# Performance work log

Hardware: AMD Instinct MI355X
Metric: run time of the kernel (lower is better)

## Reference

```python
import jax, jax.numpy as jnp
import numpy as np

B, T, D, U = 256, 2048, 64, 64


def setup_inputs() -> dict:
    key = jax.random.key(0)
    k1, k2, k3 = jax.random.split(key, 3)
    x = jax.random.normal(k1, (B, T, D), dtype=jnp.float32)
    Wx = jax.random.normal(k2, (D, 4 * U), dtype=jnp.float32) * 0.05
    Wh = jax.random.normal(k3, (U, 4 * U), dtype=jnp.float32) * 0.05
    b = jnp.zeros((4 * U,), dtype=jnp.float32)
    return {"x": x, "Wx": Wx, "Wh": Wh, "b": b}


def reference(x, Wx, Wh, b):
    # Keras LSTM gate order: i, f, g(candidate), o; act=tanh, rec_act=sigmoid.
    u = Wh.shape[0]
    # Precompute the input projection for all timesteps (same math, vectorized).
    xz = jnp.einsum('btd,dg->btg', x, Wx) + b  # [B, T, 4U]

    def step(carry, zt):
        h, c = carry                       # [B, U] each
        z = zt + h @ Wh                    # [B, 4U]
        i = jax.nn.sigmoid(z[:, :u])
        f = jax.nn.sigmoid(z[:, u:2 * u])
        g = jnp.tanh(z[:, 2 * u:3 * u])
        o = jax.nn.sigmoid(z[:, 3 * u:])
        c_new = f * c + i * g
        h_new = o * jnp.tanh(c_new)
        return (h_new, c_new), (c_new, h_new)

    h0 = jnp.zeros((x.shape[0], u), dtype=x.dtype)
    c0 = jnp.zeros((x.shape[0], u), dtype=x.dtype)
    _, (cs, hs) = jax.lax.scan(step, (h0, c0), jnp.swapaxes(xz, 0, 1))
    cs = jnp.swapaxes(cs, 0, 1)  # [B, T, U]
    hs = jnp.swapaxes(hs, 0, 1)  # [B, T, U]
    return jnp.concatenate([cs, hs], axis=-1)  # [B, T, 2U], cell states first
```

## Files before the change

### kernel.cpp

```cpp
#include <hip/hip_runtime.h>
#include <stdint.h>


#define T_STEPS 2048
#define DIM     64
#define GATES   256
#define CHUNK   16
#define NCHUNK  (T_STEPS / CHUNK)

typedef _Float16 f16;
typedef _Float16 f16x8 __attribute__((ext_vector_type(8)));
typedef float    f32x4 __attribute__((ext_vector_type(4)));

__device__ __forceinline__ void sync_lds() {
    __builtin_amdgcn_sched_barrier(0);
    asm volatile("s_waitcnt lgkmcnt(0)" ::: "memory");
    __builtin_amdgcn_sched_barrier(0);
    __builtin_amdgcn_s_barrier();
    __builtin_amdgcn_sched_barrier(0);
}

__device__ __forceinline__ float sigm(float z) {
    return __builtin_amdgcn_rcpf(1.f + __expf(-z));
}

#define MFMA16(A, B, C) __builtin_amdgcn_mfma_f32_16x16x32_f16(A, B, C, 0, 0, 0)

__device__ __forceinline__ void pack8(f16x8& d, const float4& a, const float4& b) {
    d[0]=(f16)a.x; d[1]=(f16)a.y; d[2]=(f16)a.z; d[3]=(f16)a.w;
    d[4]=(f16)b.x; d[5]=(f16)b.y; d[6]=(f16)b.z; d[7]=(f16)b.w;
}

__global__ __launch_bounds__(256, 1)
void lstm_r13_kernel(const float* __restrict__ x,
                     const float* __restrict__ Wx,
                     const float* __restrict__ Wh,
                     const float* __restrict__ bias,
                     float* __restrict__ out)
{
    __shared__ __align__(16) f16   sH[2][64];
    __shared__ __align__(16) float sXZ[4][CHUNK][16][4];

    const int tid  = threadIdx.x;
    const int lane = tid & 63;
    const int w    = tid >> 6;
    const int j    = lane & 15;
    const int g    = lane >> 4;
    const int u    = w * 16 + j;

    const int batch = blockIdx.x;
    const float* xb = x + (size_t)batch * T_STEPS * DIM;
    float* ob = out + (size_t)batch * T_STEPS * (2 * DIM);

    f16x8 Bh[4][2], Bx[4][2];
    f32x4 bias4[4];
#pragma unroll
    for (int q = 0; q < 4; ++q) {
        const int col = q * 64 + u;
        const float bb = bias[col];
        bias4[q][0] = bb; bias4[q][1] = bb; bias4[q][2] = bb; bias4[q][3] = bb;
#pragma unroll
        for (int ks = 0; ks < 2; ++ks)
#pragma unroll
            for (int e = 0; e < 8; ++e) {
                const int k = ks * 32 + g * 8 + e;
                Bh[q][ks][e] = (f16)Wh[k * GATES + col];
                Bx[q][ks][e] = (f16)Wx[k * GATES + col];
            }
    }
    const f32x4 zero4 = {0.f, 0.f, 0.f, 0.f};

    if (tid < 128) sH[tid >> 6][tid & 63] = (f16)0.f;

    float4 x0, x1, x2, x3;
    {
        const float* xr = xb + (size_t)j * DIM + g * 8;
        x0 = *(const float4*)(xr);      x1 = *(const float4*)(xr + 4);
        x2 = *(const float4*)(xr + 32); x3 = *(const float4*)(xr + 36);
    }

    float c = 0.f;
    __syncthreads();

#pragma unroll 1
    for (int n = 0; n < NCHUNK; ++n) {
        f16x8 ax0, ax1;
        pack8(ax0, x0, x1); pack8(ax1, x2, x3);
        f32x4 z0 = MFMA16(ax0, Bx[0][0], bias4[0]); z0 = MFMA16(ax1, Bx[0][1], z0);
        f32x4 z1 = MFMA16(ax0, Bx[1][0], bias4[1]); z1 = MFMA16(ax1, Bx[1][1], z1);
        f32x4 z2 = MFMA16(ax0, Bx[2][0], bias4[2]); z2 = MFMA16(ax1, Bx[2][1], z2);
        f32x4 z3 = MFMA16(ax0, Bx[3][0], bias4[3]); z3 = MFMA16(ax1, Bx[3][1], z3);
#pragma unroll
        for (int r = 0; r < 4; ++r) {
            float4 v = {z0[r], z1[r], z2[r], z3[r]};
            *(float4*)&sXZ[w][4 * g + r][j][0] = v;
        }
        asm volatile("s_waitcnt lgkmcnt(0)" ::: "memory");

        if (n + 1 < NCHUNK) {
            const float* xr = xb + ((size_t)(n + 1) * CHUNK + j) * DIM + g * 8;
            x0 = *(const float4*)(xr);      x1 = *(const float4*)(xr + 4);
            x2 = *(const float4*)(xr + 32); x3 = *(const float4*)(xr + 36);
        }

#pragma unroll
        for (int s = 0; s < CHUNK; ++s) {
            const int pb = s & 1;
            float4 xzv = *(const float4*)&sXZ[w][s][j][0];
            f16x8 A0 = *(const f16x8*)&sH[pb][g * 8];
            f16x8 A1 = *(const f16x8*)&sH[pb][32 + g * 8];

            f32x4 h0 = MFMA16(A0, Bh[0][0], zero4); h0 = MFMA16(A1, Bh[0][1], h0);
            f32x4 h1 = MFMA16(A0, Bh[1][0], zero4); h1 = MFMA16(A1, Bh[1][1], h1);
            f32x4 h2 = MFMA16(A0, Bh[2][0], zero4); h2 = MFMA16(A1, Bh[2][1], h2);
            f32x4 h3 = MFMA16(A0, Bh[3][0], zero4); h3 = MFMA16(A1, Bh[3][1], h3);

            float zi = h0[0] + xzv.x, zf = h1[0] + xzv.y;
            float zg = h2[0] + xzv.z, zo = h3[0] + xzv.w;
            float gi = sigm(zi), gf = sigm(zf), go = sigm(zo);
            float gg = fmaf(2.f, sigm(zg + zg), -1.f);
            c = fmaf(gf, c, gi * gg);
            float e2 = __expf(-2.f * fabsf(c));
            float th = copysignf(
                fmaf(-2.f, e2 * __builtin_amdgcn_rcpf(1.f + e2), 1.f), c);
            float hh = go * th;

            const size_t t = (size_t)n * CHUNK + s;
            if (g == 2)      sH[pb ^ 1][u] = (f16)hh;
            else if (g == 0) ob[t * 128 + u]      = c;
            else if (g == 1) ob[t * 128 + 64 + u] = hh;
            sync_lds();
        }
    }
}

extern "C" void kernel_launch(void* const* d_in, const int* in_sizes, int n_in,
                              void* d_out, int out_size, void* d_ws, size_t ws_size,
                              hipStream_t stream) {
    const float* x  = (const float*)d_in[0];
    const float* Wx = (const float*)d_in[1];
    const float* Wh = (const float*)d_in[2];
    const float* b  = (const float*)d_in[3];
    float* out = (float*)d_out;

    hipLaunchKernelGGL(lstm_r13_kernel, dim3(256), dim3(256), 0, stream,
                       x, Wx, Wh, b, out);
}
```

Measured before the change: 586.1 us.

## Run each batch LSTM on a single wavefront to drop per-step barriers

Collapses the four-wave block into one 64-lane wave per batch row. That wave computes all 16 gate tiles of the recurrent matmul itself, keeping the Wh fragments in registers and the Wx fragments in LDS. Because only one wave is involved, the per-timestep LDS barrier disappears, and each lane selects its gate values with a lane-dependent pick. The cost is four times more serial MFMA work per step on a single wave and only one wave per CU to hide latency.

```diff
diff --git a/kernel.cpp b/kernel.cpp
--- a/kernel.cpp
+++ b/kernel.cpp
@@ -12,14 +12,6 @@
 typedef _Float16 f16x8 __attribute__((ext_vector_type(8)));
 typedef float    f32x4 __attribute__((ext_vector_type(4)));
 
-__device__ __forceinline__ void sync_lds() {
-    __builtin_amdgcn_sched_barrier(0);
-    asm volatile("s_waitcnt lgkmcnt(0)" ::: "memory");
-    __builtin_amdgcn_sched_barrier(0);
-    __builtin_amdgcn_s_barrier();
-    __builtin_amdgcn_sched_barrier(0);
-}
-
 __device__ __forceinline__ float sigm(float z) {
     return __builtin_amdgcn_rcpf(1.f + __expf(-z));
 }
@@ -31,46 +23,56 @@
     d[4]=(f16)b.x; d[5]=(f16)b.y; d[6]=(f16)b.z; d[7]=(f16)b.w;
 }
 
-__global__ __launch_bounds__(256, 1)
-void lstm_r13_kernel(const float* __restrict__ x,
+__device__ __forceinline__ float pick4(int m, float A0, float A1, float A2, float A3) {
+    float r  = (m & 1) ? A1 : A0;
+    float sx = (m & 1) ? A3 : A2;
+    return (m & 2) ? sx : r;
+}
+
+__global__ __attribute__((amdgpu_flat_work_group_size(64, 64),
+                          amdgpu_waves_per_eu(1, 1)))
+void lstm_r14_kernel(const float* __restrict__ x,
                      const float* __restrict__ Wx,
                      const float* __restrict__ Wh,
                      const float* __restrict__ bias,
                      float* __restrict__ out)
 {
     __shared__ __align__(16) f16   sH[2][64];
-    __shared__ __align__(16) float sXZ[4][CHUNK][16][4];
+    __shared__ __align__(16) f16x8 sBx[CHUNK][2][64];
+    __shared__ __align__(16) float sXZ[CHUNK][4][64];
 
-    const int tid  = threadIdx.x;
-    const int lane = tid & 63;
-    const int w    = tid >> 6;
-    const int j    = lane & 15;
-    const int g    = lane >> 4;
-    const int u    = w * 16 + j;
+    const int l = threadIdx.x;
+    const int j = l & 15;
+    const int g = l >> 4;
+    const int u = g * 16 + j;
 
     const int batch = blockIdx.x;
     const float* xb = x + (size_t)batch * T_STEPS * DIM;
     float* ob = out + (size_t)batch * T_STEPS * (2 * DIM);
 
-    f16x8 Bh[4][2], Bx[4][2];
-    f32x4 bias4[4];
+    f16x8 Bh[16][2];
 #pragma unroll
-    for (int q = 0; q < 4; ++q) {
-        const int col = q * 64 + u;
-        const float bb = bias[col];
-        bias4[q][0] = bb; bias4[q][1] = bb; bias4[q][2] = bb; bias4[q][3] = bb;
+    for (int T = 0; T < 16; ++T) {
+        const int col = 16 * T + j;
 #pragma unroll
-        for (int ks = 0; ks < 2; ++ks)
+        for (int ks = 0; ks < 2; ++ks) {
+            f16x8 bx, bh;
 #pragma unroll
             for (int e = 0; e < 8; ++e) {
                 const int k = ks * 32 + g * 8 + e;
-                Bh[q][ks][e] = (f16)Wh[k * GATES + col];
-                Bx[q][ks][e] = (f16)Wx[k * GATES + col];
+                bh[e] = (f16)Wh[k * GATES + col];
+                bx[e] = (f16)Wx[k * GATES + col];
             }
+            Bh[T][ks] = bh;
+            sBx[T][ks][l] = bx;
+        }
     }
+    const float bi = bias[u], bf = bias[64 + u], bg = bias[128 + u], bo = bias[192 + u];
+
+    sH[0][l] = (f16)0.f;
+    sH[1][l] = (f16)0.f;
+
     const f32x4 zero4 = {0.f, 0.f, 0.f, 0.f};
-
-    if (tid < 128) sH[tid >> 6][tid & 63] = (f16)0.f;
 
     float4 x0, x1, x2, x3;
     {
@@ -80,22 +82,19 @@
     }
 
     float c = 0.f;
-    __syncthreads();
 
 #pragma unroll 1
     for (int n = 0; n < NCHUNK; ++n) {
         f16x8 ax0, ax1;
         pack8(ax0, x0, x1); pack8(ax1, x2, x3);
-        f32x4 z0 = MFMA16(ax0, Bx[0][0], bias4[0]); z0 = MFMA16(ax1, Bx[0][1], z0);
-        f32x4 z1 = MFMA16(ax0, Bx[1][0], bias4[1]); z1 = MFMA16(ax1, Bx[1][1], z1);
-        f32x4 z2 = MFMA16(ax0, Bx[2][0], bias4[2]); z2 = MFMA16(ax1, Bx[2][1], z2);
-        f32x4 z3 = MFMA16(ax0, Bx[3][0], bias4[3]); z3 = MFMA16(ax1, Bx[3][1], z3);
 #pragma unroll
-        for (int r = 0; r < 4; ++r) {
-            float4 v = {z0[r], z1[r], z2[r], z3[r]};
-            *(float4*)&sXZ[w][4 * g + r][j][0] = v;
+        for (int T = 0; T < 16; ++T) {
+            f32x4 a = MFMA16(ax0, sBx[T][0][l], zero4);
+            a = MFMA16(ax1, sBx[T][1][l], a);
+#pragma unroll
+            for (int r = 0; r < 4; ++r)
+                sXZ[4 * g + r][T >> 2][(T & 3) * 16 + j] = a[r];
         }
-        asm volatile("s_waitcnt lgkmcnt(0)" ::: "memory");
 
         if (n + 1 < NCHUNK) {
             const float* xr = xb + ((size_t)(n + 1) * CHUNK + j) * DIM + g * 8;
@@ -106,17 +105,22 @@
 #pragma unroll
         for (int s = 0; s < CHUNK; ++s) {
             const int pb = s & 1;
-            float4 xzv = *(const float4*)&sXZ[w][s][j][0];
+            float xzi = sXZ[s][0][u], xzf = sXZ[s][1][u];
+            float xzg = sXZ[s][2][u], xzo = sXZ[s][3][u];
             f16x8 A0 = *(const f16x8*)&sH[pb][g * 8];
             f16x8 A1 = *(const f16x8*)&sH[pb][32 + g * 8];
 
-            f32x4 h0 = MFMA16(A0, Bh[0][0], zero4); h0 = MFMA16(A1, Bh[0][1], h0);
-            f32x4 h1 = MFMA16(A0, Bh[1][0], zero4); h1 = MFMA16(A1, Bh[1][1], h1);
-            f32x4 h2 = MFMA16(A0, Bh[2][0], zero4); h2 = MFMA16(A1, Bh[2][1], h2);
-            f32x4 h3 = MFMA16(A0, Bh[3][0], zero4); h3 = MFMA16(A1, Bh[3][1], h3);
+            f32x4 hv[16];
+#pragma unroll
+            for (int T = 0; T < 16; ++T) {
+                f32x4 a = MFMA16(A0, Bh[T][0], zero4);
+                hv[T] = MFMA16(A1, Bh[T][1], a);
+            }
+            float zi = pick4(g, hv[0][0],  hv[1][0],  hv[2][0],  hv[3][0])  + xzi + bi;
+            float zf = pick4(g, hv[4][0],  hv[5][0],  hv[6][0],  hv[7][0])  + xzf + bf;
+            float zg = pick4(g, hv[8][0],  hv[9][0],  hv[10][0], hv[11][0]) + xzg + bg;
+            float zo = pick4(g, hv[12][0], hv[13][0], hv[14][0], hv[15][0]) + xzo + bo;
 
-            float zi = h0[0] + xzv.x, zf = h1[0] + xzv.y;
-            float zg = h2[0] + xzv.z, zo = h3[0] + xzv.w;
             float gi = sigm(zi), gf = sigm(zf), go = sigm(zo);
             float gg = fmaf(2.f, sigm(zg + zg), -1.f);
             c = fmaf(gf, c, gi * gg);
@@ -125,11 +129,10 @@
                 fmaf(-2.f, e2 * __builtin_amdgcn_rcpf(1.f + e2), 1.f), c);
             float hh = go * th;
 
+            sH[pb ^ 1][u] = (f16)hh;
             const size_t t = (size_t)n * CHUNK + s;
-            if (g == 2)      sH[pb ^ 1][u] = (f16)hh;
-            else if (g == 0) ob[t * 128 + u]      = c;
-            else if (g == 1) ob[t * 128 + 64 + u] = hh;
-            sync_lds();
+            ob[t * 128 + u]      = c;
+            ob[t * 128 + 64 + u] = hh;
         }
     }
 }
@@ -143,6 +146,6 @@
     const float* b  = (const float*)d_in[3];
     float* out = (float*)d_out;
 
-    hipLaunchKernelGGL(lstm_r13_kernel, dim3(256), dim3(256), 0, stream,
+    hipLaunchKernelGGL(lstm_r14_kernel, dim3(256), dim3(64), 0, stream,
                        x, Wx, Wh, b, out);
 }
```

New measurement: 914.6 us. 1.56x slower.
